# Kernel tuning notes

Hardware: AMD Instinct MI355X
Metric: run time of the kernel (lower is better)

The kernel has to match this reference:

```python
import jax, jax.numpy as jnp
import numpy as np

XYZ_MIN = jnp.array([-1.0, -1.0, -1.0], dtype=jnp.float32)
XYZ_MAX = jnp.array([1.0, 1.0, 1.0], dtype=jnp.float32)
ALPHA_INIT = 0.01
ACT_SHIFT = float(np.log(1.0 / (1.0 - ALPHA_INIT) - 1.0))
INTERVAL = 0.5  # stepsize * voxel_size_ratio
NEAR, FAR = 0.2, 1.8
N_RAYS, N_SAMPLES = 4096, 256
GRID = 160
K0_DIM = 12
VIEW_PE = 4
WIDTH = 128
DIM0 = 3 + 3 * VIEW_PE * 2 + K0_DIM  # 39


def trilinear(grid, pts):
    """grid: [X,Y,Z,C]; pts: [N,3] world coords -> [N,C] (align_corners=True, border clamp)."""
    sz = jnp.array(grid.shape[:3], dtype=pts.dtype)
    ijk = (pts - XYZ_MIN) / (XYZ_MAX - XYZ_MIN) * (sz - 1.0)
    ijk = jnp.clip(ijk, 0.0, sz - 1.0)
    lo = jnp.clip(jnp.floor(ijk).astype(jnp.int32), 0, jnp.array(grid.shape[:3], jnp.int32) - 2)
    f = ijk - lo.astype(pts.dtype)
    hi = lo + 1
    x0, y0, z0 = lo[:, 0], lo[:, 1], lo[:, 2]
    x1, y1, z1 = hi[:, 0], hi[:, 1], hi[:, 2]
    fx, fy, fz = f[:, 0:1], f[:, 1:2], f[:, 2:3]
    c00 = grid[x0, y0, z0] * (1 - fz) + grid[x0, y0, z1] * fz
    c01 = grid[x0, y1, z0] * (1 - fz) + grid[x0, y1, z1] * fz
    c10 = grid[x1, y0, z0] * (1 - fz) + grid[x1, y0, z1] * fz
    c11 = grid[x1, y1, z0] * (1 - fz) + grid[x1, y1, z1] * fz
    c0 = c00 * (1 - fy) + c01 * fy
    c1 = c10 * (1 - fy) + c11 * fy
    return c0 * (1 - fx) + c1 * fx


def setup_inputs() -> dict:
    key = jax.random.key(0)
    ks = jax.random.split(key, 8)
    rays_o = jax.random.uniform(ks[0], (N_RAYS, 3), jnp.float32, -0.3, 0.3)
    rays_d = jax.random.normal(ks[1], (N_RAYS, 3), jnp.float32)
    density = jax.random.normal(ks[2], (GRID, GRID, GRID), jnp.float32)
    k0 = jax.random.normal(ks[3], (K0_DIM, GRID, GRID, GRID), jnp.float32) * 0.1
    W0 = jax.random.normal(ks[4], (DIM0, WIDTH), jnp.float32) * (1.0 / np.sqrt(DIM0))
    b0 = jnp.zeros((WIDTH,), jnp.float32)
    W1 = jax.random.normal(ks[5], (WIDTH, WIDTH), jnp.float32) * (1.0 / np.sqrt(WIDTH))
    b1 = jnp.zeros((WIDTH,), jnp.float32)
    W2 = jax.random.normal(ks[6], (WIDTH, 3), jnp.float32) * (1.0 / np.sqrt(WIDTH))
    b2 = jnp.zeros((3,), jnp.float32)
    return {"rays_o": rays_o, "rays_d": rays_d, "density": density, "k0": k0,
            "W0": W0, "b0": b0, "W1": W1, "b1": b1, "W2": W2, "b2": b2}


def reference(rays_o, rays_d, density, k0, W0, b0, W1, b1, W2, b2):
    R, S = rays_o.shape[0], N_SAMPLES
    viewdirs = rays_d / jnp.linalg.norm(rays_d, axis=-1, keepdims=True)
    t = jnp.linspace(NEAR, FAR, S, dtype=rays_o.dtype)  # [S]
    pts = rays_o[:, None, :] + rays_d[:, None, :] * t[None, :, None]  # [R,S,3]
    ptsf = pts.reshape(-1, 3)

    # Raw2Alpha: alpha = 1 - (1 + exp(d + shift))^(-interval)
    sigma = trilinear(density[..., None], ptsf)[:, 0].reshape(R, S)
    alpha = 1.0 - jnp.power(1.0 + jnp.exp(sigma + ACT_SHIFT), -INTERVAL)

    # Alphas2Weights: per-ray exclusive cumprod of transmittance
    Tcum = jnp.cumprod(1.0 - alpha + 1e-10, axis=1)  # [R,S]
    T = jnp.concatenate([jnp.ones((R, 1), alpha.dtype), Tcum[:, :-1]], axis=1)
    weights = alpha * T
    alphainv_last = Tcum[:, -1]

    # k0 features + view positional encoding -> rgbnet MLP
    feat = trilinear(jnp.moveaxis(k0, 0, -1), ptsf).reshape(R, S, K0_DIM)
    freq = (2.0 ** jnp.arange(VIEW_PE)).astype(rays_o.dtype)  # [P]
    vf = viewdirs[:, :, None] * freq[None, None, :]  # [R,3,P]
    vemb = jnp.concatenate([viewdirs, jnp.sin(vf).reshape(R, -1), jnp.cos(vf).reshape(R, -1)], axis=-1)  # [R,27]
    x = jnp.concatenate([feat, jnp.broadcast_to(vemb[:, None, :], (R, S, vemb.shape[-1]))], axis=-1)  # [R,S,39]

    h = jax.nn.relu(x @ W0 + b0)
    h = jax.nn.relu(h @ W1 + b1)
    rgb = jax.nn.sigmoid(h @ W2 + b2)  # [R,S,3]

    # composite with white background
    rgb_marched = jnp.sum(weights[..., None] * rgb, axis=1) + alphainv_last[:, None]
    return rgb_marched
```

## Files before the change

### kernel.cpp

```cpp
#include <hip/hip_runtime.h>
#include <hip/hip_bf16.h>

#define NRAYS 4096
#define NS 256
#define G 160
#define G2 (160*160)
#define G3 (160*160*160)
#define K0DIM 12
#define WIDTH 128
#define CHUNK 32
#define NCHUNK 8
#define HBS 136
#define ACT_SHIFT_F (-4.5951198501345889f)
#define TNEAR 0.2f
#define TFAR 1.8f

typedef unsigned short u16;
typedef unsigned int u32;
typedef __attribute__((ext_vector_type(8))) short short8;
typedef __attribute__((ext_vector_type(4))) float floatx4;

#define W1F_IDX(kq, qs, n) (((((kq)<<2) + (qs)) * 128 + (n)) << 3)

__device__ __forceinline__ float bf2f(u16 u) {
    union { u32 i; float f; } v; v.i = ((u32)u) << 16; return v.f;
}
__device__ __forceinline__ u16 f2bf(float f) {
    union { float f; u32 u; } v; v.f = f;
    u32 r = v.u + 0x7FFFu + ((v.u >> 16) & 1u);
    return (u16)(r >> 16);
}

__device__ __forceinline__ float loadv(const float* p, int i) { return p[i]; }
__device__ __forceinline__ float loadv(const u16* p, int i)   { return bf2f(p[i]); }
__device__ __forceinline__ void storev(float* p, int i, float v) { p[i] = v; }
__device__ __forceinline__ void storev(u16* p, int i, float v)   { p[i] = f2bf(v); }

template <typename T> struct QT;
template <> struct QT<u16>   { using type = ushort4; };
template <> struct QT<float> { using type = float4;  };

__device__ __forceinline__ void zpair(const ushort4& q, int d, float& v0, float& v1) {
    u16 r0 = (d == 0) ? q.x : ((d == 1) ? q.y : q.z);
    u16 r1 = (d == 0) ? q.y : ((d == 1) ? q.z : q.w);
    v0 = bf2f(r0); v1 = bf2f(r1);
}
__device__ __forceinline__ void zpair(const float4& q, int d, float& v0, float& v1) {
    v0 = (d == 0) ? q.x : ((d == 1) ? q.y : q.z);
    v1 = (d == 0) ? q.y : ((d == 1) ? q.z : q.w);
}

struct CoordsE { int base; int d; float fx, fy, fz; };

__device__ __forceinline__ CoordsE coords_e(float px, float py, float pz) {
    float gx = fminf(fmaxf((px + 1.0f) * 79.5f, 0.0f), 159.0f);
    float gy = fminf(fmaxf((py + 1.0f) * 79.5f, 0.0f), 159.0f);
    float gz = fminf(fmaxf((pz + 1.0f) * 79.5f, 0.0f), 159.0f);
    int ix = (int)gx; if (ix > 158) ix = 158;
    int iy = (int)gy; if (iy > 158) iy = 158;
    int iz = (int)gz; if (iz > 158) iz = 158;
    int ze = iz & ~1; if (ze > 156) ze = 156;
    CoordsE c;
    c.base = (ix * G + iy) * G + ze;
    c.d = iz - ze;
    c.fx = gx - (float)ix; c.fy = gy - (float)iy; c.fz = gz - (float)iz;
    return c;
}

__global__ void decide_mode(const u16* __restrict__ rays_d_u16, int* __restrict__ mode) {
    if (blockIdx.x == 0 && threadIdx.x == 0) {
        int bad = 0;
        for (int i = 0; i < 128; i++) {
            u16 u = rays_d_u16[i];
            int e = (u >> 7) & 0xFF;
            int m = u & 0x7F;
            float v = bf2f(u);
            if (e == 0xFF || (e == 0 && m != 0) || fabsf(v) > 32.0f) bad++;
        }
        *mode = (bad >= 4) ? 1 : 0;
    }
}

template <typename T, typename OT, int MODE>
__global__ __launch_bounds__(256, 3)
void dvgo_fused(const T* __restrict__ rays_o, const T* __restrict__ rays_d,
                const T* __restrict__ density, const T* __restrict__ k0,
                const T* __restrict__ W0, const T* __restrict__ b0,
                const T* __restrict__ W1, const T* __restrict__ b1,
                const T* __restrict__ W2, const T* __restrict__ b2,
                OT* __restrict__ out, const int* __restrict__ mode)
{
    if (*mode != MODE) return;

    using qvec = typename QT<T>::type;

    __shared__ __align__(16) u16   W1f[WIDTH * WIDTH];
    __shared__ __align__(16) u16   h0B[CHUNK * HBS];
    __shared__ __align__(16) u16   W0f[WIDTH * 16];
    __shared__ __align__(16) u16   featB[CHUNK * 16];
    __shared__ __align__(16) float W2Tf[3 * WIDTH];
    __shared__ float p2[CHUNK * 6];
    __shared__ float base0[WIDTH];
    __shared__ float b1s[WIDTH];
    __shared__ float b2s[3];
    __shared__ float vembs[27];
    __shared__ float wts[NS];
    __shared__ float red[96];
    __shared__ float ainvs;

    const int r = blockIdx.x;
    const int tid = threadIdx.x;

    const float o0 = loadv(rays_o, r*3+0);
    const float o1 = loadv(rays_o, r*3+1);
    const float o2 = loadv(rays_o, r*3+2);
    const float d0 = loadv(rays_d, r*3+0);
    const float d1 = loadv(rays_d, r*3+1);
    const float d2 = loadv(rays_d, r*3+2);

    for (int idx = tid; idx < WIDTH*WIDTH; idx += 256) {
        int k = idx >> 7, n = idx & 127;
        W1f[W1F_IDX(k >> 5, (k >> 3) & 3, n) + (k & 7)] = f2bf(loadv(W1, idx));
    }
    for (int i = tid; i < WIDTH*16; i += 256) {
        int n = i >> 4, k = i & 15;
        W0f[i] = (k < K0DIM) ? f2bf(loadv(W0, k*WIDTH + n)) : (u16)0;
    }
    for (int i = tid; i < CHUNK*4; i += 256)
        featB[(i >> 2)*16 + 12 + (i & 3)] = 0;
    for (int k = tid; k < 3*WIDTH; k += 256) {
        int c = k >> 7, i = k & 127;
        W2Tf[k] = loadv(W2, i*3 + c);
    }
    if (tid < WIDTH) b1s[tid] = loadv(b1, tid);
    if (tid < 3)     b2s[tid] = loadv(b2, tid);

    if (tid < 27) {
        float inv = rsqrtf(d0*d0 + d1*d1 + d2*d2);
        float v0 = d0*inv, v1 = d1*inv, v2 = d2*inv;
        float val;
        if (tid < 3) {
            val = (tid == 0) ? v0 : ((tid == 1) ? v1 : v2);
        } else if (tid < 15) {
            int t2 = tid - 3; int dd = t2 >> 2; int p = t2 & 3;
            float vd = (dd == 0) ? v0 : ((dd == 1) ? v1 : v2);
            val = sinf(vd * (float)(1 << p));
        } else {
            int t2 = tid - 15; int dd = t2 >> 2; int p = t2 & 3;
            float vd = (dd == 0) ? v0 : ((dd == 1) ? v1 : v2);
            val = cosf(vd * (float)(1 << p));
        }
        vembs[tid] = val;
    }
    __syncthreads();

    if (tid < WIDTH) {
        float a = loadv(b0, tid);
        #pragma unroll
        for (int i = 0; i < 27; i++)
            a += vembs[i] * loadv(W0, (K0DIM + i)*WIDTH + tid);
        base0[tid] = a;
    }

    {
        int s = tid;
        float tv = TNEAR + (TFAR - TNEAR) * ((float)s * (1.0f/(float)(NS-1)));
        CoordsE c = coords_e(o0 + d0*tv, o1 + d1*tv, o2 + d2*tv);
        qvec q00 = *(const qvec*)(density + c.base);
        qvec q01 = *(const qvec*)(density + c.base + G);
        qvec q10 = *(const qvec*)(density + c.base + G2);
        qvec q11 = *(const qvec*)(density + c.base + G2 + G);
        float a0,a1,b0v,b1v,c0v,c1v,d0v,d1v;
        zpair(q00, c.d, a0, a1); zpair(q01, c.d, b0v, b1v);
        zpair(q10, c.d, c0v, c1v); zpair(q11, c.d, d0v, d1v);
        float c00 = a0*(1.0f-c.fz) + a1*c.fz;
        float c01 = b0v*(1.0f-c.fz) + b1v*c.fz;
        float c10 = c0v*(1.0f-c.fz) + c1v*c.fz;
        float c11 = d0v*(1.0f-c.fz) + d1v*c.fz;
        float e0 = c00*(1.0f-c.fy) + c01*c.fy;
        float e1 = c10*(1.0f-c.fy) + c11*c.fy;
        float sigma = e0*(1.0f-c.fx) + e1*c.fx;
        float alpha = 1.0f - rsqrtf(1.0f + __expf(sigma + ACT_SHIFT_F));
        wts[s] = alpha;
    }
    __syncthreads();

    if (tid == 0) {
        float w = 1.0f;
        for (int s = 0; s < NS; s++) {
            float a = wts[s];
            wts[s] = a * w;
            w *= (1.0f - a + 1e-10f);
        }
        ainvs = w;
    }
    __syncthreads();

    const int lane = tid & 63;
    const int wvid = tid >> 6;
    const int mt   = wvid & 1;
    const int nh   = wvid >> 1;
    const int q    = lane >> 4;
    const int ncol = lane & 15;
    const int arow = mt*16 + ncol;
    const int kcol = q * 8;
    const int drow0 = mt*16 + q*4;

    qvec qa[4], qb[4];
    CoordsE cea, ceb;
    const int ch0 = tid >> 5;
    const int sl0 = tid & 31;
    const int ch1 = 8 + (tid >> 5);
    const int sl1 = tid & 31;
    const bool has1 = (tid < 128);

    #define ISSUE_GATHER(CH, SL, C0N, Q, CE)                                    \
        { int s_ = (C0N) + (SL);                                                \
          float tv_ = TNEAR + (TFAR - TNEAR) * ((float)s_ * (1.0f/255.0f));     \
          CE = coords_e(o0 + d0*tv_, o1 + d1*tv_, o2 + d2*tv_);                 \
          const T* g_ = k0 + (size_t)(CH)*G3;                                   \
          Q[0] = *(const qvec*)(g_ + CE.base);                                  \
          Q[1] = *(const qvec*)(g_ + CE.base + G);                              \
          Q[2] = *(const qvec*)(g_ + CE.base + G2);                             \
          Q[3] = *(const qvec*)(g_ + CE.base + G2 + G); }

    #define COMMIT_GATHER(CH, SL, Q, CE)                                        \
        { float a0_,a1_,b0_,b1_,c0_,c1_,d0_,d1_;                                \
          zpair(Q[0], CE.d, a0_, a1_); zpair(Q[1], CE.d, b0_, b1_);             \
          zpair(Q[2], CE.d, c0_, c1_); zpair(Q[3], CE.d, d0_, d1_);             \
          float fz_ = CE.fz, fy_ = CE.fy, fx_ = CE.fx;                          \
          float c00_ = a0_*(1.0f-fz_) + a1_*fz_;                                \
          float c01_ = b0_*(1.0f-fz_) + b1_*fz_;                                \
          float c10_ = c0_*(1.0f-fz_) + c1_*fz_;                                \
          float c11_ = d0_*(1.0f-fz_) + d1_*fz_;                                \
          float e0_ = c00_*(1.0f-fy_) + c01_*fy_;                               \
          float e1_ = c10_*(1.0f-fy_) + c11_*fy_;                               \
          featB[(SL)*16 + (CH)] = f2bf(e0_*(1.0f-fx_) + e1_*fx_); }

    ISSUE_GATHER(ch0, sl0, 0, qa, cea);
    if (has1) ISSUE_GATHER(ch1, sl1, 0, qb, ceb);

    float rgbacc = 0.0f;

    for (int cc = 0; cc < NCHUNK; cc++) {
        const int c0 = cc * CHUNK;

        COMMIT_GATHER(ch0, sl0, qa, cea);
        if (has1) COMMIT_GATHER(ch1, sl1, qb, ceb);
        __syncthreads();

        {
            short8 af0 = {};
            short8 bf0 = {}, bf1 = {}, bf2v = {}, bf3 = {};
            if (q < 2) {
                af0  = *(const short8*)&featB[arow*16 + kcol];
                bf0  = *(const short8*)&W0f[(nh*64 +  0 + ncol)*16 + kcol];
                bf1  = *(const short8*)&W0f[(nh*64 + 16 + ncol)*16 + kcol];
                bf2v = *(const short8*)&W0f[(nh*64 + 32 + ncol)*16 + kcol];
                bf3  = *(const short8*)&W0f[(nh*64 + 48 + ncol)*16 + kcol];
            }
            floatx4 acc0[4];
            #pragma unroll
            for (int t = 0; t < 4; t++) {
                float v = base0[nh*64 + t*16 + ncol];
                acc0[t] = (floatx4){v, v, v, v};
            }
            acc0[0] = __builtin_amdgcn_mfma_f32_16x16x32_bf16(af0, bf0,  acc0[0], 0, 0, 0);
            acc0[1] = __builtin_amdgcn_mfma_f32_16x16x32_bf16(af0, bf1,  acc0[1], 0, 0, 0);
            acc0[2] = __builtin_amdgcn_mfma_f32_16x16x32_bf16(af0, bf2v, acc0[2], 0, 0, 0);
            acc0[3] = __builtin_amdgcn_mfma_f32_16x16x32_bf16(af0, bf3,  acc0[3], 0, 0, 0);
            #pragma unroll
            for (int t = 0; t < 4; t++) {
                int j = nh*64 + t*16 + ncol;
                #pragma unroll
                for (int rI = 0; rI < 4; rI++)
                    h0B[(drow0 + rI)*HBS + j] = f2bf(fmaxf(acc0[t][rI], 0.0f));
            }
        }
        __syncthreads();

        if (cc + 1 < NCHUNK) {
            ISSUE_GATHER(ch0, sl0, c0 + CHUNK, qa, cea);
            if (has1) ISSUE_GATHER(ch1, sl1, c0 + CHUNK, qb, ceb);
        }

        {
            floatx4 acc[4];
            #pragma unroll
            for (int t = 0; t < 4; t++) {
                float bj = b1s[nh*64 + t*16 + ncol];
                acc[t] = (floatx4){bj, bj, bj, bj};
            }
            #pragma unroll
            for (int kq = 0; kq < 4; kq++) {
                short8 af = *(const short8*)&h0B[arow*HBS + kq*32 + kcol];
                #pragma unroll
                for (int t = 0; t < 4; t++) {
                    short8 bf = *(const short8*)&W1f[W1F_IDX(kq, q, nh*64 + t*16 + ncol)];
                    acc[t] = __builtin_amdgcn_mfma_f32_16x16x32_bf16(af, bf, acc[t], 0, 0, 0);
                }
            }

            float p[3][4];
            #pragma unroll
            for (int c = 0; c < 3; c++)
                { p[c][0]=0; p[c][1]=0; p[c][2]=0; p[c][3]=0; }
            #pragma unroll
            for (int t = 0; t < 4; t++) {
                int j = nh*64 + t*16 + ncol;
                float w20 = W2Tf[j], w21 = W2Tf[WIDTH + j], w22 = W2Tf[2*WIDTH + j];
                #pragma unroll
                for (int rI = 0; rI < 4; rI++) {
                    float h = fmaxf(acc[t][rI], 0.0f);
                    p[0][rI] += h * w20;
                    p[1][rI] += h * w21;
                    p[2][rI] += h * w22;
                }
            }
            #pragma unroll
            for (int m = 1; m <= 8; m <<= 1) {
                #pragma unroll
                for (int c = 0; c < 3; c++) {
                    #pragma unroll
                    for (int rI = 0; rI < 4; rI++)
                        p[c][rI] += __shfl_xor(p[c][rI], m, 64);
                }
            }
            if (ncol == 0) {
                #pragma unroll
                for (int rI = 0; rI < 4; rI++) {
                    #pragma unroll
                    for (int c = 0; c < 3; c++)
                        p2[(drow0 + rI)*6 + nh*3 + c] = p[c][rI];
                }
            }
        }
        __syncthreads();

        if (tid < 96) {
            int c = tid >> 5, s = tid & 31;
            float acc2 = b2s[c] + p2[s*6 + c] + p2[s*6 + 3 + c];
            float rgb = 1.0f / (1.0f + __expf(-acc2));
            rgbacc += wts[c0 + s] * rgb;
        }
    }

    if (tid < 96) red[tid] = rgbacc;
    __syncthreads();
    if (tid < 3) {
        float s = 0.0f;
        #pragma unroll
        for (int k = 0; k < 32; k++) s += red[tid*32 + k];
        storev(out, r*3 + tid, s + ainvs);
    }
    #undef ISSUE_GATHER
    #undef COMMIT_GATHER
}

extern "C" void kernel_launch(void* const* d_in, const int* in_sizes, int n_in,
                              void* d_out, int out_size, void* d_ws, size_t ws_size,
                              hipStream_t stream) {
    int* mode = (int*)d_ws;
    decide_mode<<<dim3(1), dim3(64), 0, stream>>>((const u16*)d_in[1], mode);

    dvgo_fused<u16, u16, 0><<<dim3(NRAYS), dim3(256), 0, stream>>>(
        (const u16*)d_in[0], (const u16*)d_in[1], (const u16*)d_in[2],
        (const u16*)d_in[3], (const u16*)d_in[4], (const u16*)d_in[5],
        (const u16*)d_in[6], (const u16*)d_in[7], (const u16*)d_in[8],
        (const u16*)d_in[9], (u16*)d_out, mode);

    dvgo_fused<float, float, 1><<<dim3(NRAYS), dim3(256), 0, stream>>>(
        (const float*)d_in[0], (const float*)d_in[1], (const float*)d_in[2],
        (const float*)d_in[3], (const float*)d_in[4], (const float*)d_in[5],
        (const float*)d_in[6], (const float*)d_in[7], (const float*)d_in[8],
        (const float*)d_in[9], (float*)d_out, mode);
}
```

Before: 522.4 us.

## Prepack MLP weights once into workspace, read from global; parallel-scan transmittance

Adds a pre-kernel that converts and swizzles W1 and W0 into bf16 MFMA layout in workspace. The fused kernel then reads these operands straight from global/L2 instead of rebuilding a 32KB LDS copy in every block, which frees LDS and raises the occupancy hint from 3 to 6 blocks per CU. The serial single-thread transmittance cumprod is replaced with a wave-level shuffle prefix-product scan. In exchange, every MFMA B-operand load now goes through the cache hierarchy instead of LDS, and the scan changes floating-point product ordering slightly.

```diff
diff --git a/kernel.cpp b/kernel.cpp
--- a/kernel.cpp
+++ b/kernel.cpp
@@ -15,6 +15,9 @@
 #define TNEAR 0.2f
 #define TFAR 1.8f
 
+#define WS_W1G_OFF 1024
+#define WS_W0G_OFF (1024 + 32768)
+
 typedef unsigned short u16;
 typedef unsigned int u32;
 typedef __attribute__((ext_vector_type(8))) short short8;
@@ -81,22 +84,39 @@
     }
 }
 
+__global__ void pack_weights(const void* __restrict__ W1, const void* __restrict__ W0,
+                             u16* __restrict__ w1g, u16* __restrict__ w0g,
+                             const int* __restrict__ mode) {
+    const int m = *mode;
+    const int idx = blockIdx.x * 256 + threadIdx.x;
+    for (int i = idx; i < WIDTH * WIDTH; i += 64 * 256) {
+        int k = i >> 7, n = i & 127;
+        float v = m ? ((const float*)W1)[i] : bf2f(((const u16*)W1)[i]);
+        w1g[W1F_IDX(k >> 5, (k >> 3) & 3, n) + (k & 7)] = f2bf(v);
+    }
+    for (int i = idx; i < WIDTH * 16; i += 64 * 256) {
+        int n = i >> 4, k = i & 15;
+        float v = 0.0f;
+        if (k < K0DIM) v = m ? ((const float*)W0)[k * WIDTH + n] : bf2f(((const u16*)W0)[k * WIDTH + n]);
+        w0g[i] = f2bf(v);
+    }
+}
+
 template <typename T, typename OT, int MODE>
-__global__ __launch_bounds__(256, 3)
+__global__ __launch_bounds__(256, 6)
 void dvgo_fused(const T* __restrict__ rays_o, const T* __restrict__ rays_d,
                 const T* __restrict__ density, const T* __restrict__ k0,
                 const T* __restrict__ W0, const T* __restrict__ b0,
                 const T* __restrict__ W1, const T* __restrict__ b1,
                 const T* __restrict__ W2, const T* __restrict__ b2,
+                const u16* __restrict__ w1g, const u16* __restrict__ w0g,
                 OT* __restrict__ out, const int* __restrict__ mode)
 {
     if (*mode != MODE) return;
 
     using qvec = typename QT<T>::type;
 
-    __shared__ __align__(16) u16   W1f[WIDTH * WIDTH];
     __shared__ __align__(16) u16   h0B[CHUNK * HBS];
-    __shared__ __align__(16) u16   W0f[WIDTH * 16];
     __shared__ __align__(16) u16   featB[CHUNK * 16];
     __shared__ __align__(16) float W2Tf[3 * WIDTH];
     __shared__ float p2[CHUNK * 6];
@@ -118,14 +138,6 @@
     const float d1 = loadv(rays_d, r*3+1);
     const float d2 = loadv(rays_d, r*3+2);
 
-    for (int idx = tid; idx < WIDTH*WIDTH; idx += 256) {
-        int k = idx >> 7, n = idx & 127;
-        W1f[W1F_IDX(k >> 5, (k >> 3) & 3, n) + (k & 7)] = f2bf(loadv(W1, idx));
-    }
-    for (int i = tid; i < WIDTH*16; i += 256) {
-        int n = i >> 4, k = i & 15;
-        W0f[i] = (k < K0DIM) ? f2bf(loadv(W0, k*WIDTH + n)) : (u16)0;
-    }
     for (int i = tid; i < CHUNK*4; i += 256)
         featB[(i >> 2)*16 + 12 + (i & 3)] = 0;
     for (int k = tid; k < 3*WIDTH; k += 256) {
@@ -185,14 +197,26 @@
     }
     __syncthreads();
 
-    if (tid == 0) {
-        float w = 1.0f;
-        for (int s = 0; s < NS; s++) {
-            float a = wts[s];
-            wts[s] = a * w;
-            w *= (1.0f - a + 1e-10f);
-        }
-        ainvs = w;
+    if (tid < 64) {
+        const int l = tid;
+        float a0 = wts[4*l+0], a1 = wts[4*l+1], a2 = wts[4*l+2], a3 = wts[4*l+3];
+        float m0 = 1.0f - a0 + 1e-10f;
+        float m1 = 1.0f - a1 + 1e-10f;
+        float m2 = 1.0f - a2 + 1e-10f;
+        float m3 = 1.0f - a3 + 1e-10f;
+        float sc = (m0*m1)*(m2*m3);
+        #pragma unroll
+        for (int dlt = 1; dlt < 64; dlt <<= 1) {
+            float o = __shfl_up(sc, dlt, 64);
+            if (l >= dlt) sc *= o;
+        }
+        float Tr = __shfl_up(sc, 1, 64);
+        if (l == 0) Tr = 1.0f;
+        wts[4*l+0] = a0 * Tr; Tr *= m0;
+        wts[4*l+1] = a1 * Tr; Tr *= m1;
+        wts[4*l+2] = a2 * Tr; Tr *= m2;
+        wts[4*l+3] = a3 * Tr; Tr *= m3;
+        if (l == 63) ainvs = Tr;
     }
     __syncthreads();
 
@@ -213,16 +237,18 @@
     const int ch1 = 8 + (tid >> 5);
     const int sl1 = tid & 31;
     const bool has1 = (tid < 128);
-
-    #define ISSUE_GATHER(CH, SL, C0N, Q, CE)                                    \
+    const u32 chb0 = (u32)ch0 * (u32)G3;
+    const u32 chb1 = (u32)ch1 * (u32)G3;
+
+    #define ISSUE_GATHER(CHB, SL, C0N, Q, CE)                                   \
         { int s_ = (C0N) + (SL);                                                \
           float tv_ = TNEAR + (TFAR - TNEAR) * ((float)s_ * (1.0f/255.0f));     \
           CE = coords_e(o0 + d0*tv_, o1 + d1*tv_, o2 + d2*tv_);                 \
-          const T* g_ = k0 + (size_t)(CH)*G3;                                   \
-          Q[0] = *(const qvec*)(g_ + CE.base);                                  \
-          Q[1] = *(const qvec*)(g_ + CE.base + G);                              \
-          Q[2] = *(const qvec*)(g_ + CE.base + G2);                             \
-          Q[3] = *(const qvec*)(g_ + CE.base + G2 + G); }
+          const T* g_ = k0 + ((CHB) + (u32)CE.base);                            \
+          Q[0] = *(const qvec*)(g_);                                            \
+          Q[1] = *(const qvec*)(g_ + G);                                        \
+          Q[2] = *(const qvec*)(g_ + G2);                                       \
+          Q[3] = *(const qvec*)(g_ + G2 + G); }
 
     #define COMMIT_GATHER(CH, SL, Q, CE)                                        \
         { float a0_,a1_,b0_,b1_,c0_,c1_,d0_,d1_;                                \
@@ -237,8 +263,8 @@
           float e1_ = c10_*(1.0f-fy_) + c11_*fy_;                               \
           featB[(SL)*16 + (CH)] = f2bf(e0_*(1.0f-fx_) + e1_*fx_); }
 
-    ISSUE_GATHER(ch0, sl0, 0, qa, cea);
-    if (has1) ISSUE_GATHER(ch1, sl1, 0, qb, ceb);
+    ISSUE_GATHER(chb0, sl0, 0, qa, cea);
+    if (has1) ISSUE_GATHER(chb1, sl1, 0, qb, ceb);
 
     float rgbacc = 0.0f;
 
@@ -254,10 +280,11 @@
             short8 bf0 = {}, bf1 = {}, bf2v = {}, bf3 = {};
             if (q < 2) {
                 af0  = *(const short8*)&featB[arow*16 + kcol];
-                bf0  = *(const short8*)&W0f[(nh*64 +  0 + ncol)*16 + kcol];
-                bf1  = *(const short8*)&W0f[(nh*64 + 16 + ncol)*16 + kcol];
-                bf2v = *(const short8*)&W0f[(nh*64 + 32 + ncol)*16 + kcol];
-                bf3  = *(const short8*)&W0f[(nh*64 + 48 + ncol)*16 + kcol];
+                const u16* wp = w0g + ((nh*64 + ncol) << 4) + kcol;
+                bf0  = *(const short8*)(wp);
+                bf1  = *(const short8*)(wp + (16 << 4));
+                bf2v = *(const short8*)(wp + (32 << 4));
+                bf3  = *(const short8*)(wp + (48 << 4));
             }
             floatx4 acc0[4];
             #pragma unroll
@@ -280,8 +307,8 @@
         __syncthreads();
 
         if (cc + 1 < NCHUNK) {
-            ISSUE_GATHER(ch0, sl0, c0 + CHUNK, qa, cea);
-            if (has1) ISSUE_GATHER(ch1, sl1, c0 + CHUNK, qb, ceb);
+            ISSUE_GATHER(chb0, sl0, c0 + CHUNK, qa, cea);
+            if (has1) ISSUE_GATHER(chb1, sl1, c0 + CHUNK, qb, ceb);
         }
 
         {
@@ -291,12 +318,14 @@
                 float bj = b1s[nh*64 + t*16 + ncol];
                 acc[t] = (floatx4){bj, bj, bj, bj};
             }
+            const u16* w1p = w1g + ((q*128 + nh*64 + ncol) << 3);
             #pragma unroll
             for (int kq = 0; kq < 4; kq++) {
                 short8 af = *(const short8*)&h0B[arow*HBS + kq*32 + kcol];
+                const u16* wk = w1p + (kq << 12);
                 #pragma unroll
                 for (int t = 0; t < 4; t++) {
-                    short8 bf = *(const short8*)&W1f[W1F_IDX(kq, q, nh*64 + t*16 + ncol)];
+                    short8 bf = *(const short8*)(wk + (t << 7));
                     acc[t] = __builtin_amdgcn_mfma_f32_16x16x32_bf16(af, bf, acc[t], 0, 0, 0);
                 }
             }
@@ -361,17 +390,21 @@
                               void* d_out, int out_size, void* d_ws, size_t ws_size,
                               hipStream_t stream) {
     int* mode = (int*)d_ws;
+    u16* w1g = (u16*)((char*)d_ws + WS_W1G_OFF);
+    u16* w0g = (u16*)((char*)d_ws + WS_W0G_OFF);
+
     decide_mode<<<dim3(1), dim3(64), 0, stream>>>((const u16*)d_in[1], mode);
+    pack_weights<<<dim3(64), dim3(256), 0, stream>>>(d_in[6], d_in[4], w1g, w0g, mode);
 
     dvgo_fused<u16, u16, 0><<<dim3(NRAYS), dim3(256), 0, stream>>>(
         (const u16*)d_in[0], (const u16*)d_in[1], (const u16*)d_in[2],
         (const u16*)d_in[3], (const u16*)d_in[4], (const u16*)d_in[5],
         (const u16*)d_in[6], (const u16*)d_in[7], (const u16*)d_in[8],
-        (const u16*)d_in[9], (u16*)d_out, mode);
+        (const u16*)d_in[9], w1g, w0g, (u16*)d_out, mode);
 
     dvgo_fused<float, float, 1><<<dim3(NRAYS), dim3(256), 0, stream>>>(
         (const float*)d_in[0], (const float*)d_in[1], (const float*)d_in[2],
         (const float*)d_in[3], (const float*)d_in[4], (const float*)d_in[5],
         (const float*)d_in[6], (const float*)d_in[7], (const float*)d_in[8],
-        (const float*)d_in[9], (float*)d_out, mode);
-}
+        (const float*)d_in[9], w1g, w0g, (float*)d_out, mode);
+}
```

Result: slower. 1.542 ms (+195.1%).
